# Kernel optimization log

Hardware: AMD Instinct MI355X
Metric: run time of the kernel (lower is better)

Reference implementation:

```python
import jax, jax.numpy as jnp
import numpy as np

B, T, C = 16, 1024, 128  # batch, block_size (window length), n_hembd


def setup_inputs() -> dict:
    key = jax.random.key(0)
    k1, k2, k3 = jax.random.split(key, 3)
    Q = jax.random.normal(k1, (B, T, C), dtype=jnp.float32)
    K = jax.random.normal(k2, (B, 2 * T - 1, C), dtype=jnp.float32)
    # learned parameter keyWindowBias: (1, 1, n_hembd, block_size)
    bias = jax.random.normal(k3, (1, 1, C, T), dtype=jnp.float32)
    return {"Q": Q, "K": K, "bias": bias}


def reference(Q, K, bias):
    # Original: K_sw = K.unfold(1, T, 1) -> (B, T, C, T) with K_sw[b,w,c,t] = K[b,w+t,c]
    #           Z = einsum('bwc,bwct->bwt', Q, K_sw + bias)
    # Distribute the dot product over the bias add to avoid materializing (B,T,C,T):
    #   Z[b,w,t] = sum_c Q[b,w,c] * K[b,w+t,c]  +  sum_c Q[b,w,c] * bias[c,t]
    Bn, Tn, Cn = Q.shape
    # Dense scores against all 2T-1 key positions: (B, T, 2T-1)
    S = jnp.einsum('bwc,bkc->bwk', Q, K)
    # Gather sliding-window diagonals: idx[w, t] = w + t
    idx = jnp.arange(Tn)[:, None] + jnp.arange(Tn)[None, :]  # (T, T)
    Zk = jnp.take_along_axis(S, idx[None, :, :], axis=2)      # (B, T, T)
    # Bias contribution: Q @ bias, shared across windows
    Zb = jnp.einsum('bwc,ct->bwt', Q, bias[0, 0])             # (B, T, T)
    return Zk + Zb
```

## Files before the change

kernel.cpp:

```cpp
#include <hip/hip_runtime.h>
#include <hip/hip_bf16.h>


#define B_    16
#define T_    1024
#define C_    128
#define KT_   2047

#define BW    32
#define BT    64
#define KROWS 96
#define SS_LD 98
#define LDB   136

#define LDSS  130

typedef unsigned short ushort_t;
typedef short bf16x8 __attribute__((ext_vector_type(8)));
typedef float f32x4  __attribute__((ext_vector_type(4)));

__device__ __forceinline__ unsigned short f2bf(float f) {
  unsigned int u = __float_as_uint(f);
  u += 0x7FFFu + ((u >> 16) & 1u);
  return (unsigned short)(u >> 16);
}

__device__ __forceinline__ bf16x8 pack8(float4 lo, float4 hi) {
  bf16x8 r;
  r[0] = (short)f2bf(lo.x); r[1] = (short)f2bf(lo.y);
  r[2] = (short)f2bf(lo.z); r[3] = (short)f2bf(lo.w);
  r[4] = (short)f2bf(hi.x); r[5] = (short)f2bf(hi.y);
  r[6] = (short)f2bf(hi.z); r[7] = (short)f2bf(hi.w);
  return r;
}

typedef const __attribute__((address_space(1))) unsigned int* gas_ptr;
typedef __attribute__((address_space(3))) unsigned int* las_ptr;
__device__ __forceinline__ void async_copy16(const void* g, void* l) {
  __builtin_amdgcn_global_load_lds((gas_ptr)g, (las_ptr)l, 16, 0, 0);
}

__device__ __forceinline__ const bf16x8* frag(const ushort_t* t, int row, int kc) {
  return (const bf16x8*)(t + (((row << 4) + (kc ^ (row & 7))) << 3));
}

#define KN4 1048064
#define BN4 32768

__global__ __launch_bounds__(256) void prepass(
    const float* __restrict__ K, const float* __restrict__ bias,
    ushort_t* __restrict__ Kb, ushort_t* __restrict__ bT) {
  int idx = blockIdx.x * 256 + threadIdx.x;
  if (idx < KN4) {
    float4 v = ((const float4*)K)[idx];
    ((ushort4*)Kb)[idx] = make_ushort4(f2bf(v.x), f2bf(v.y), f2bf(v.z), f2bf(v.w));
  } else {
    int i = idx - KN4;
    int c = i >> 8;
    int g = i & 255;
    float4 v = ((const float4*)(bias + c * T_))[g];
    int t = g << 2;
    bT[(t + 0) * C_ + c] = f2bf(v.x);
    bT[(t + 1) * C_ + c] = f2bf(v.y);
    bT[(t + 2) * C_ + c] = f2bf(v.z);
    bT[(t + 3) * C_ + c] = f2bf(v.w);
  }
}

__global__ __launch_bounds__(512) void swmm_main(
    const float* __restrict__ Q, const ushort_t* __restrict__ Kb,
    const ushort_t* __restrict__ bT, float* __restrict__ out) {
  __shared__ __align__(16) ushort_t tile[5120 * 8];
  __shared__ __align__(16) float Ss[64 * LDSS];

  const int b    = blockIdx.x;
  const int w0   = blockIdx.y * 64;
  const int tid  = threadIdx.x;
  const int wv   = tid >> 6;
  const int lane = tid & 63;
  const int frow = lane & 15;
  const int quad = lane >> 4;
  const int jb   = wv & 3;
  const int mg   = wv >> 2;

  const int r0 = tid >> 4;
  const int cc = (tid & 15) ^ (r0 & 7);
  const ushort_t* kbb = Kb + (size_t)b * KT_ * C_ + (cc << 3);
  const ushort_t* btb = bT + (cc << 3);

  auto stageK = [&](int chunk, int p) {
    int g0 = w0 + chunk * 64 + r0;
    int g1 = g0 + 32;
    if (g1 > KT_ - 1) g1 = KT_ - 1;
    async_copy16(kbb + (size_t)g0 * C_, &tile[(size_t)(p * 1024 + wv * 64) * 8]);
    async_copy16(kbb + (size_t)g1 * C_, &tile[(size_t)(p * 1024 + 512 + wv * 64) * 8]);
  };
  auto stageB = [&](int step, int q) {
    const ushort_t* g = btb + (size_t)(step * 64 + r0) * C_;
    async_copy16(g,           &tile[(size_t)(3072 + q * 1024 + wv * 64) * 8]);
    async_copy16(g + 32 * C_, &tile[(size_t)(3072 + q * 1024 + 512 + wv * 64) * 8]);
  };

  stageK(0, 0); stageK(1, 1); stageB(0, 0);

  bf16x8 a[4][4];
  {
    const float* qp = Q + ((size_t)(b * T_ + w0 + frow) << 7);
#pragma unroll
    for (int mi = 0; mi < 4; ++mi) {
      const float* qm = qp + ((size_t)(mi * 16) << 7);
#pragma unroll
      for (int kk = 0; kk < 4; ++kk) {
        int co = (kk * 4 + quad) << 3;
        float4 lo = *(const float4*)(qm + co);
        float4 hi = *(const float4*)(qm + co + 4);
        a[mi][kk] = pack8(lo, hi);
      }
    }
  }

  asm volatile("s_waitcnt vmcnt(0)" ::: "memory");
  __builtin_amdgcn_s_barrier();

  int p0 = 0, p1 = 1, p2 = 2;
  f32x4 baccA = {0.f, 0.f, 0.f, 0.f}, baccB = {0.f, 0.f, 0.f, 0.f};

  for (int s = 0; s < 16; ++s) {
    const int q0 = s & 1;

    if (s < 15) stageK(s + 2, p2);
    if (s < 15) stageB(s + 1, q0 ^ 1);

    __builtin_amdgcn_s_setprio(1);

    {
      const int n0 = wv * 16;
      const int pc = (wv >= 4) ? p1 : p0;
      const int lrow = pc * 64 + ((n0 + frow) & 63);
      f32x4 acc[4];
#pragma unroll
      for (int mi = 0; mi < 4; ++mi) acc[mi] = (f32x4){0.f, 0.f, 0.f, 0.f};
#pragma unroll
      for (int kk = 0; kk < 4; ++kk) {
        bf16x8 bb = *frag(tile, lrow, kk * 4 + quad);
#pragma unroll
        for (int mi = 0; mi < 4; ++mi)
          acc[mi] = __builtin_amdgcn_mfma_f32_16x16x32_bf16(a[mi][kk], bb, acc[mi], 0, 0, 0);
      }
#pragma unroll
      for (int mi = 0; mi < 4; ++mi)
#pragma unroll
        for (int r = 0; r < 4; ++r)
          Ss[(mi * 16 + quad * 4 + r) * LDSS + n0 + frow] = acc[mi][r];
    }

    {
      const int brow = 192 + q0 * 64 + jb * 16 + frow;
      f32x4 xA = {0.f, 0.f, 0.f, 0.f};
      f32x4 xB = {0.f, 0.f, 0.f, 0.f};
#pragma unroll
      for (int kk = 0; kk < 4; ++kk) {
        bf16x8 bb = *frag(tile, brow, kk * 4 + quad);
        xA = __builtin_amdgcn_mfma_f32_16x16x32_bf16(a[2 * mg + 0][kk], bb, xA, 0, 0, 0);
        xB = __builtin_amdgcn_mfma_f32_16x16x32_bf16(a[2 * mg + 1][kk], bb, xB, 0, 0, 0);
      }
      baccA = xA; baccB = xB;
    }

    __builtin_amdgcn_s_setprio(0);

    asm volatile("s_waitcnt lgkmcnt(0)" ::: "memory");
    __builtin_amdgcn_s_barrier();
    asm volatile("s_waitcnt vmcnt(0)" ::: "memory");

    {
      float* op = out + ((size_t)(b * T_ + w0) * T_) + s * 64 + jb * 16 + frow;
#pragma unroll
      for (int pi = 0; pi < 2; ++pi) {
        const int mi = 2 * mg + pi;
        const f32x4 acc = pi ? baccB : baccA;
#pragma unroll
        for (int r = 0; r < 4; ++r) {
          const int i = mi * 16 + quad * 4 + r;
          op[(size_t)i * T_] = acc[r] + Ss[i * LDSS + i + jb * 16 + frow];
        }
      }
    }
    asm volatile("s_waitcnt lgkmcnt(0)" ::: "memory");
    __builtin_amdgcn_s_barrier();

    const int tp = p0; p0 = p1; p1 = p2; p2 = tp;
  }
}

__global__ __launch_bounds__(256) void swmm_fallback(
    const float* __restrict__ Q, const float* __restrict__ K,
    const float* __restrict__ bias, float* __restrict__ out) {
  __shared__ __align__(16) unsigned short Qs[BW * LDB];
  __shared__ __align__(16) unsigned short Ks[KROWS * LDB];
  __shared__ __align__(16) unsigned short Bs[BT * LDB];
  __shared__ __align__(16) float Ssf[BW * SS_LD];

  const int b   = blockIdx.z;
  const int w0  = blockIdx.y * BW;
  const int t0  = blockIdx.x * BT;
  const int kbase = w0 + t0;
  const int tid = threadIdx.x;

  {
    const float4* src = (const float4*)(Q + (size_t)(b * T_ + w0) * C_);
    for (int v = tid; v < BW * (C_ / 4); v += 256) {
      int r = v >> 5, cc = v & 31;
      float4 q = src[r * 32 + cc];
      unsigned short* d = &Qs[r * LDB + (cc << 2)];
      d[0] = f2bf(q.x); d[1] = f2bf(q.y); d[2] = f2bf(q.z); d[3] = f2bf(q.w);
    }
  }
  {
    for (int v = tid; v < KROWS * (C_ / 4); v += 256) {
      int r = v >> 5, cc = v & 31;
      int g = kbase + r;
      float4 kv = make_float4(0.f, 0.f, 0.f, 0.f);
      if (g < KT_) kv = ((const float4*)(K + ((size_t)b * KT_ + g) * C_))[cc];
      unsigned short* d = &Ks[r * LDB + (cc << 2)];
      d[0] = f2bf(kv.x); d[1] = f2bf(kv.y); d[2] = f2bf(kv.z); d[3] = f2bf(kv.w);
    }
  }
  {
    for (int v = tid; v < C_ * (BT / 4); v += 256) {
      int c = v >> 4, jj = v & 15;
      float4 bv = ((const float4*)(bias + (size_t)c * T_ + t0))[jj];
      int j4 = jj << 2;
      Bs[(j4 + 0) * LDB + c] = f2bf(bv.x);
      Bs[(j4 + 1) * LDB + c] = f2bf(bv.y);
      Bs[(j4 + 2) * LDB + c] = f2bf(bv.z);
      Bs[(j4 + 3) * LDB + c] = f2bf(bv.w);
    }
  }
  __syncthreads();

  const int wv    = tid >> 6;
  const int lane  = tid & 63;
  const int frow  = lane & 15;
  const int koff  = (lane >> 4) * 8;
  const int drow4 = (lane >> 4) * 4;
  const int NS = KROWS / 16;

  for (int s = wv; s < 2 * NS; s += 4) {
    int mb = s / NS, nn = s % NS;
    int m0 = mb * 16, n0 = nn * 16;
    const unsigned short* arow = &Qs[(m0 + frow) * LDB + koff];
    const unsigned short* brow = &Ks[(n0 + frow) * LDB + koff];
    f32x4 acc = {0.f, 0.f, 0.f, 0.f};
#pragma unroll
    for (int k0 = 0; k0 < C_; k0 += 32) {
      bf16x8 a  = *(const bf16x8*)(arow + k0);
      bf16x8 bb = *(const bf16x8*)(brow + k0);
      acc = __builtin_amdgcn_mfma_f32_16x16x32_bf16(a, bb, acc, 0, 0, 0);
    }
#pragma unroll
    for (int r = 0; r < 4; ++r)
      Ssf[(m0 + drow4 + r) * SS_LD + n0 + frow] = acc[r];
  }

  f32x4 bacc[2];
#pragma unroll
  for (int q = 0; q < 2; ++q) {
    int idx = wv + q * 4;
    int m0 = (idx >> 2) * 16, jj0 = (idx & 3) * 16;
    const unsigned short* arow = &Qs[(m0 + frow) * LDB + koff];
    const unsigned short* brow = &Bs[(jj0 + frow) * LDB + koff];
    f32x4 acc = {0.f, 0.f, 0.f, 0.f};
#pragma unroll
    for (int k0 = 0; k0 < C_; k0 += 32) {
      bf16x8 a  = *(const bf16x8*)(arow + k0);
      bf16x8 bb = *(const bf16x8*)(brow + k0);
      acc = __builtin_amdgcn_mfma_f32_16x16x32_bf16(a, bb, acc, 0, 0, 0);
    }
    bacc[q] = acc;
  }
  __syncthreads();

#pragma unroll
  for (int q = 0; q < 2; ++q) {
    int idx = wv + q * 4;
    int m0 = (idx >> 2) * 16, jj0 = (idx & 3) * 16;
#pragma unroll
    for (int r = 0; r < 4; ++r) {
      int i = m0 + drow4 + r;
      int j = jj0 + frow;
      out[(size_t)(b * T_ + w0 + i) * T_ + t0 + j] = bacc[q][r] + Ssf[i * SS_LD + i + j];
    }
  }
}

extern "C" void kernel_launch(void* const* d_in, const int* in_sizes, int n_in,
                              void* d_out, int out_size, void* d_ws, size_t ws_size,
                              hipStream_t stream) {
  const float* Q    = (const float*)d_in[0];
  const float* K    = (const float*)d_in[1];
  const float* bias = (const float*)d_in[2];
  float* out = (float*)d_out;

  const size_t KB = (size_t)B_ * KT_ * C_ * 2;
  const size_t TB = (size_t)T_ * C_ * 2;

  if (ws_size >= KB + TB) {
    ushort_t* Kb = (ushort_t*)d_ws;
    ushort_t* bT = (ushort_t*)((char*)d_ws + KB);
    prepass<<<(KN4 + BN4) / 256, 256, 0, stream>>>(K, bias, Kb, bT);
    swmm_main<<<dim3(B_, T_ / 64), dim3(512), 0, stream>>>(Q, Kb, bT, out);
  } else {
    swmm_fallback<<<dim3(T_ / BT, T_ / BW, B_), dim3(256), 0, stream>>>(Q, K, bias, out);
  }
}
```

Baseline: 129.4 us.

## Stage bias scores in LDS for vectorized output stores and loosen vmcnt waits

The bias MFMA results are written to a new shared buffer, so each thread can emit contiguous float4 stores of 8 output values per row instead of scattered per-lane scalar stores. The wait on global loads moves to the top of each step using a partial vmcnt, which lets prefetches stay in flight across iterations, and the trailing barrier is removed. The intent is wider, coalesced output writes and better overlap of loads with compute. The cost is extra LDS traffic and footprint, plus a reliance on vmcnt counting, since the output stores also increment vmcnt, and on removing the final barrier, both of which risk correctness or hazards.

```diff
diff --git a/kernel.cpp b/kernel.cpp
--- a/kernel.cpp
+++ b/kernel.cpp
@@ -14,6 +14,7 @@
 #define LDB   136
 
 #define LDSS  130
+#define LDBS  65
 
 typedef unsigned short ushort_t;
 typedef short bf16x8 __attribute__((ext_vector_type(8)));
@@ -72,6 +73,7 @@
     const ushort_t* __restrict__ bT, float* __restrict__ out) {
   __shared__ __align__(16) ushort_t tile[5120 * 8];
   __shared__ __align__(16) float Ss[64 * LDSS];
+  __shared__ __align__(16) float Bss[64 * LDBS];
 
   const int b    = blockIdx.x;
   const int w0   = blockIdx.y * 64;
@@ -119,20 +121,25 @@
     }
   }
 
-  asm volatile("s_waitcnt vmcnt(0)" ::: "memory");
-  __builtin_amdgcn_s_barrier();
+  const int pi_row = tid >> 3;
+  const int pj0    = (tid & 7) * 8;
+  float* outb = out + ((size_t)(b * T_ + w0 + pi_row) * T_) + pj0;
 
   int p0 = 0, p1 = 1, p2 = 2;
-  f32x4 baccA = {0.f, 0.f, 0.f, 0.f}, baccB = {0.f, 0.f, 0.f, 0.f};
 
   for (int s = 0; s < 16; ++s) {
     const int q0 = s & 1;
 
-    if (s < 15) stageK(s + 2, p2);
-    if (s < 15) stageB(s + 1, q0 ^ 1);
+    if (s < 15) {
+      stageK(s + 2, p2);
+      stageB(s + 1, q0 ^ 1);
+    }
+    if (s < 15) asm volatile("s_waitcnt vmcnt(4)" ::: "memory");
+    else        asm volatile("s_waitcnt vmcnt(0)" ::: "memory");
+    __builtin_amdgcn_s_barrier();
+    __builtin_amdgcn_sched_barrier(0);
 
     __builtin_amdgcn_s_setprio(1);
-
     {
       const int n0 = wv * 16;
       const int pc = (wv >= 4) ? p1 : p0;
@@ -153,7 +160,6 @@
         for (int r = 0; r < 4; ++r)
           Ss[(mi * 16 + quad * 4 + r) * LDSS + n0 + frow] = acc[mi][r];
     }
-
     {
       const int brow = 192 + q0 * 64 + jb * 16 + frow;
       f32x4 xA = {0.f, 0.f, 0.f, 0.f};
@@ -164,30 +170,29 @@
         xA = __builtin_amdgcn_mfma_f32_16x16x32_bf16(a[2 * mg + 0][kk], bb, xA, 0, 0, 0);
         xB = __builtin_amdgcn_mfma_f32_16x16x32_bf16(a[2 * mg + 1][kk], bb, xB, 0, 0, 0);
       }
-      baccA = xA; baccB = xB;
-    }
-
+#pragma unroll
+      for (int r = 0; r < 4; ++r) {
+        Bss[((2 * mg + 0) * 16 + quad * 4 + r) * LDBS + jb * 16 + frow] = xA[r];
+        Bss[((2 * mg + 1) * 16 + quad * 4 + r) * LDBS + jb * 16 + frow] = xB[r];
+      }
+    }
     __builtin_amdgcn_s_setprio(0);
 
     asm volatile("s_waitcnt lgkmcnt(0)" ::: "memory");
     __builtin_amdgcn_s_barrier();
-    asm volatile("s_waitcnt vmcnt(0)" ::: "memory");
+    __builtin_amdgcn_sched_barrier(0);
 
     {
-      float* op = out + ((size_t)(b * T_ + w0) * T_) + s * 64 + jb * 16 + frow;
-#pragma unroll
-      for (int pi = 0; pi < 2; ++pi) {
-        const int mi = 2 * mg + pi;
-        const f32x4 acc = pi ? baccB : baccA;
-#pragma unroll
-        for (int r = 0; r < 4; ++r) {
-          const int i = mi * 16 + quad * 4 + r;
-          op[(size_t)i * T_] = acc[r] + Ss[i * LDSS + i + jb * 16 + frow];
-        }
-      }
+      float v[8];
+      const float* srow = &Ss[pi_row * LDSS + pi_row + pj0];
+      const float* brow2 = &Bss[pi_row * LDBS + pj0];
+#pragma unroll
+      for (int k = 0; k < 8; ++k) v[k] = srow[k] + brow2[k];
+      float4* dst = (float4*)(outb + (size_t)s * 64);
+      dst[0] = make_float4(v[0], v[1], v[2], v[3]);
+      dst[1] = make_float4(v[4], v[5], v[6], v[7]);
     }
     asm volatile("s_waitcnt lgkmcnt(0)" ::: "memory");
-    __builtin_amdgcn_s_barrier();
 
     const int tp = p0; p0 = p1; p1 = p2; p2 = tp;
   }
```

After: 147.9 us. 1.14x slower.

## Replace pipelined persistent-row kernel with small one-shot tiles and bf16 Q prepass

Applied to the files above, without the earlier changes.

The main kernel no longer has each 512-thread block walk all 16 t-chunks of a 64-row window with a triple-buffered async pipeline. Each 256-thread block now handles a 32x64 output tile: it loads Q, a 96-row K band and 64 bias rows in one async batch, runs both MFMA products, and writes the diagonal-gathered sum with float4 stores. Q is also converted to bf16 in the prepass, which adds one more global round trip. Blocks become shorter and far more numerous, giving better occupancy, but K and Q are reloaded per tile and there is no longer any load/compute overlap inside a block.

```diff
diff --git a/kernel.cpp b/kernel.cpp
--- a/kernel.cpp
+++ b/kernel.cpp
@@ -11,9 +11,7 @@
 #define BT    64
 #define KROWS 96
 #define SS_LD 98
-#define LDB   136
-
-#define LDSS  130
+#define LDBS2 68
 
 typedef unsigned short ushort_t;
 typedef short bf16x8 __attribute__((ext_vector_type(8)));
@@ -25,15 +23,6 @@
   return (unsigned short)(u >> 16);
 }
 
-__device__ __forceinline__ bf16x8 pack8(float4 lo, float4 hi) {
-  bf16x8 r;
-  r[0] = (short)f2bf(lo.x); r[1] = (short)f2bf(lo.y);
-  r[2] = (short)f2bf(lo.z); r[3] = (short)f2bf(lo.w);
-  r[4] = (short)f2bf(hi.x); r[5] = (short)f2bf(hi.y);
-  r[6] = (short)f2bf(hi.z); r[7] = (short)f2bf(hi.w);
-  return r;
-}
-
 typedef const __attribute__((address_space(1))) unsigned int* gas_ptr;
 typedef __attribute__((address_space(3))) unsigned int* las_ptr;
 __device__ __forceinline__ void async_copy16(const void* g, void* l) {
@@ -44,18 +33,24 @@
   return (const bf16x8*)(t + (((row << 4) + (kc ^ (row & 7))) << 3));
 }
 
+#define QN4 524288
 #define KN4 1048064
 #define BN4 32768
 
 __global__ __launch_bounds__(256) void prepass(
-    const float* __restrict__ K, const float* __restrict__ bias,
+    const float* __restrict__ Q, const float* __restrict__ K,
+    const float* __restrict__ bias, ushort_t* __restrict__ Qb,
     ushort_t* __restrict__ Kb, ushort_t* __restrict__ bT) {
   int idx = blockIdx.x * 256 + threadIdx.x;
-  if (idx < KN4) {
-    float4 v = ((const float4*)K)[idx];
-    ((ushort4*)Kb)[idx] = make_ushort4(f2bf(v.x), f2bf(v.y), f2bf(v.z), f2bf(v.w));
-  } else {
-    int i = idx - KN4;
+  if (idx < QN4) {
+    float4 v = ((const float4*)Q)[idx];
+    ((ushort4*)Qb)[idx] = make_ushort4(f2bf(v.x), f2bf(v.y), f2bf(v.z), f2bf(v.w));
+  } else if (idx < QN4 + KN4) {
+    int i = idx - QN4;
+    float4 v = ((const float4*)K)[i];
+    ((ushort4*)Kb)[i] = make_ushort4(f2bf(v.x), f2bf(v.y), f2bf(v.z), f2bf(v.w));
+  } else if (idx < QN4 + KN4 + BN4) {
+    int i = idx - (QN4 + KN4);
     int c = i >> 8;
     int g = i & 255;
     float4 v = ((const float4*)(bias + c * T_))[g];
@@ -67,132 +62,104 @@
   }
 }
 
-__global__ __launch_bounds__(512) void swmm_main(
-    const float* __restrict__ Q, const ushort_t* __restrict__ Kb,
+__global__ __launch_bounds__(256) void swmm_main(
+    const ushort_t* __restrict__ Qb, const ushort_t* __restrict__ Kb,
     const ushort_t* __restrict__ bT, float* __restrict__ out) {
-  __shared__ __align__(16) ushort_t tile[5120 * 8];
-  __shared__ __align__(16) float Ss[64 * LDSS];
-
-  const int b    = blockIdx.x;
-  const int w0   = blockIdx.y * 64;
-  const int tid  = threadIdx.x;
-  const int wv   = tid >> 6;
-  const int lane = tid & 63;
+  __shared__ __align__(16) ushort_t tile[3072 * 8];
+
+  const int b  = blockIdx.z;
+  const int w0 = blockIdx.y * BW;
+  const int t0 = blockIdx.x * BT;
+  const int kbase = w0 + t0;
+  const int tid = threadIdx.x;
+  const int wv = tid >> 6, lane = tid & 63;
+
+#pragma unroll
+  for (int seg = 0; seg < 12; ++seg) {
+    int slot = seg * 256 + tid;
+    int r = slot >> 4;
+    int c = (slot & 15) ^ (r & 7);
+    const ushort_t* g;
+    if (seg < 2) {
+      g = Qb + (((size_t)(b * T_ + w0 + r)) << 7) + (c << 3);
+    } else if (seg < 8) {
+      int gk = kbase + (r - 32);
+      if (gk > KT_ - 1) gk = KT_ - 1;
+      g = Kb + ((size_t)b * KT_ + gk) * C_ + (c << 3);
+    } else {
+      g = bT + (((size_t)(t0 + r - 128)) << 7) + (c << 3);
+    }
+    async_copy16(g, &tile[(size_t)(seg * 256 + wv * 64) * 8]);
+  }
+  __syncthreads();
+
   const int frow = lane & 15;
   const int quad = lane >> 4;
-  const int jb   = wv & 3;
-  const int mg   = wv >> 2;
-
-  const int r0 = tid >> 4;
-  const int cc = (tid & 15) ^ (r0 & 7);
-  const ushort_t* kbb = Kb + (size_t)b * KT_ * C_ + (cc << 3);
-  const ushort_t* btb = bT + (cc << 3);
-
-  auto stageK = [&](int chunk, int p) {
-    int g0 = w0 + chunk * 64 + r0;
-    int g1 = g0 + 32;
-    if (g1 > KT_ - 1) g1 = KT_ - 1;
-    async_copy16(kbb + (size_t)g0 * C_, &tile[(size_t)(p * 1024 + wv * 64) * 8]);
-    async_copy16(kbb + (size_t)g1 * C_, &tile[(size_t)(p * 1024 + 512 + wv * 64) * 8]);
-  };
-  auto stageB = [&](int step, int q) {
-    const ushort_t* g = btb + (size_t)(step * 64 + r0) * C_;
-    async_copy16(g,           &tile[(size_t)(3072 + q * 1024 + wv * 64) * 8]);
-    async_copy16(g + 32 * C_, &tile[(size_t)(3072 + q * 1024 + 512 + wv * 64) * 8]);
-  };
-
-  stageK(0, 0); stageK(1, 1); stageB(0, 0);
-
-  bf16x8 a[4][4];
-  {
-    const float* qp = Q + ((size_t)(b * T_ + w0 + frow) << 7);
-#pragma unroll
-    for (int mi = 0; mi < 4; ++mi) {
-      const float* qm = qp + ((size_t)(mi * 16) << 7);
-#pragma unroll
-      for (int kk = 0; kk < 4; ++kk) {
-        int co = (kk * 4 + quad) << 3;
-        float4 lo = *(const float4*)(qm + co);
-        float4 hi = *(const float4*)(qm + co + 4);
-        a[mi][kk] = pack8(lo, hi);
-      }
-    }
-  }
-
-  asm volatile("s_waitcnt vmcnt(0)" ::: "memory");
-  __builtin_amdgcn_s_barrier();
-
-  int p0 = 0, p1 = 1, p2 = 2;
-  f32x4 baccA = {0.f, 0.f, 0.f, 0.f}, baccB = {0.f, 0.f, 0.f, 0.f};
-
-  for (int s = 0; s < 16; ++s) {
-    const int q0 = s & 1;
-
-    if (s < 15) stageK(s + 2, p2);
-    if (s < 15) stageB(s + 1, q0 ^ 1);
-
-    __builtin_amdgcn_s_setprio(1);
-
-    {
-      const int n0 = wv * 16;
-      const int pc = (wv >= 4) ? p1 : p0;
-      const int lrow = pc * 64 + ((n0 + frow) & 63);
-      f32x4 acc[4];
-#pragma unroll
-      for (int mi = 0; mi < 4; ++mi) acc[mi] = (f32x4){0.f, 0.f, 0.f, 0.f};
-#pragma unroll
-      for (int kk = 0; kk < 4; ++kk) {
-        bf16x8 bb = *frag(tile, lrow, kk * 4 + quad);
-#pragma unroll
-        for (int mi = 0; mi < 4; ++mi)
-          acc[mi] = __builtin_amdgcn_mfma_f32_16x16x32_bf16(a[mi][kk], bb, acc[mi], 0, 0, 0);
-      }
-#pragma unroll
-      for (int mi = 0; mi < 4; ++mi)
-#pragma unroll
-        for (int r = 0; r < 4; ++r)
-          Ss[(mi * 16 + quad * 4 + r) * LDSS + n0 + frow] = acc[mi][r];
-    }
-
-    {
-      const int brow = 192 + q0 * 64 + jb * 16 + frow;
-      f32x4 xA = {0.f, 0.f, 0.f, 0.f};
-      f32x4 xB = {0.f, 0.f, 0.f, 0.f};
-#pragma unroll
-      for (int kk = 0; kk < 4; ++kk) {
-        bf16x8 bb = *frag(tile, brow, kk * 4 + quad);
-        xA = __builtin_amdgcn_mfma_f32_16x16x32_bf16(a[2 * mg + 0][kk], bb, xA, 0, 0, 0);
-        xB = __builtin_amdgcn_mfma_f32_16x16x32_bf16(a[2 * mg + 1][kk], bb, xB, 0, 0, 0);
-      }
-      baccA = xA; baccB = xB;
-    }
-
-    __builtin_amdgcn_s_setprio(0);
-
-    asm volatile("s_waitcnt lgkmcnt(0)" ::: "memory");
-    __builtin_amdgcn_s_barrier();
-    asm volatile("s_waitcnt vmcnt(0)" ::: "memory");
-
-    {
-      float* op = out + ((size_t)(b * T_ + w0) * T_) + s * 64 + jb * 16 + frow;
-#pragma unroll
-      for (int pi = 0; pi < 2; ++pi) {
-        const int mi = 2 * mg + pi;
-        const f32x4 acc = pi ? baccB : baccA;
-#pragma unroll
-        for (int r = 0; r < 4; ++r) {
-          const int i = mi * 16 + quad * 4 + r;
-          op[(size_t)i * T_] = acc[r] + Ss[i * LDSS + i + jb * 16 + frow];
-        }
-      }
-    }
-    asm volatile("s_waitcnt lgkmcnt(0)" ::: "memory");
-    __builtin_amdgcn_s_barrier();
-
-    const int tp = p0; p0 = p1; p1 = p2; p2 = tp;
-  }
-}
-
+  const int drow4 = quad * 4;
+
+  f32x4 bacc[2];
+#pragma unroll
+  for (int q = 0; q < 2; ++q) {
+    int idx = wv + q * 4;
+    int m0 = (idx >> 2) * 16, j0 = (idx & 3) * 16;
+    f32x4 acc = {0.f, 0.f, 0.f, 0.f};
+#pragma unroll
+    for (int kk = 0; kk < 4; ++kk) {
+      int kc = kk * 4 + quad;
+      bf16x8 a  = *frag(tile, m0 + frow, kc);
+      bf16x8 bb = *frag(tile, 128 + j0 + frow, kc);
+      acc = __builtin_amdgcn_mfma_f32_16x16x32_bf16(a, bb, acc, 0, 0, 0);
+    }
+    bacc[q] = acc;
+  }
+  __syncthreads();
+
+  float* Ss = (float*)&tile[2048 * 8];
+#pragma unroll
+  for (int q = 0; q < 3; ++q) {
+    int s = wv + q * 4;
+    int mb = s / 6, nn = s % 6;
+    int m0 = mb * 16, n0 = nn * 16;
+    f32x4 acc = {0.f, 0.f, 0.f, 0.f};
+#pragma unroll
+    for (int kk = 0; kk < 4; ++kk) {
+      int kc = kk * 4 + quad;
+      bf16x8 a  = *frag(tile, m0 + frow, kc);
+      bf16x8 bb = *frag(tile, 32 + n0 + frow, kc);
+      acc = __builtin_amdgcn_mfma_f32_16x16x32_bf16(a, bb, acc, 0, 0, 0);
+    }
+#pragma unroll
+    for (int r = 0; r < 4; ++r)
+      Ss[(m0 + drow4 + r) * SS_LD + n0 + frow] = acc[r];
+  }
+  __syncthreads();
+
+  float* Bss = (float*)&tile[4096];
+#pragma unroll
+  for (int q = 0; q < 2; ++q) {
+    int idx = wv + q * 4;
+    int m0 = (idx >> 2) * 16, j0 = (idx & 3) * 16;
+#pragma unroll
+    for (int r = 0; r < 4; ++r)
+      Bss[(m0 + drow4 + r) * LDBS2 + j0 + frow] = bacc[q][r];
+  }
+  __syncthreads();
+
+  {
+    const int pi  = tid >> 3;
+    const int pj0 = (tid & 7) * 8;
+    float v[8];
+    const float* srow = &Ss[pi * SS_LD + pi + pj0];
+    const float* brow = &Bss[pi * LDBS2 + pj0];
+#pragma unroll
+    for (int k = 0; k < 8; ++k) v[k] = srow[k] + brow[k];
+    float4* dst = (float4*)(out + (size_t)(b * T_ + w0 + pi) * T_ + t0 + pj0);
+    dst[0] = make_float4(v[0], v[1], v[2], v[3]);
+    dst[1] = make_float4(v[4], v[5], v[6], v[7]);
+  }
+}
+
+#define LDB 136
 __global__ __launch_bounds__(256) void swmm_fallback(
     const float* __restrict__ Q, const float* __restrict__ K,
     const float* __restrict__ bias, float* __restrict__ out) {
@@ -267,9 +234,9 @@
 #pragma unroll
   for (int q = 0; q < 2; ++q) {
     int idx = wv + q * 4;
-    int m0 = (idx >> 2) * 16, jj0 = (idx & 3) * 16;
+    int m0 = (idx >> 2) * 16, j0 = (idx & 3) * 16;
     const unsigned short* arow = &Qs[(m0 + frow) * LDB + koff];
-    const unsigned short* brow = &Bs[(jj0 + frow) * LDB + koff];
+    const unsigned short* brow = &Bs[(j0 + frow) * LDB + koff];
     f32x4 acc = {0.f, 0.f, 0.f, 0.f};
 #pragma unroll
     for (int k0 = 0; k0 < C_; k0 += 32) {
@@ -284,11 +251,11 @@
 #pragma unroll
   for (int q = 0; q < 2; ++q) {
     int idx = wv + q * 4;
-    int m0 = (idx >> 2) * 16, jj0 = (idx & 3) * 16;
+    int m0 = (idx >> 2) * 16, j0 = (idx & 3) * 16;
 #pragma unroll
     for (int r = 0; r < 4; ++r) {
       int i = m0 + drow4 + r;
-      int j = jj0 + frow;
+      int j = j0 + frow;
       out[(size_t)(b * T_ + w0 + i) * T_ + t0 + j] = bacc[q][r] + Ssf[i * SS_LD + i + j];
     }
   }
@@ -302,15 +269,18 @@
   const float* bias = (const float*)d_in[2];
   float* out = (float*)d_out;
 
+  const size_t QB = (size_t)B_ * T_ * C_ * 2;
   const size_t KB = (size_t)B_ * KT_ * C_ * 2;
   const size_t TB = (size_t)T_ * C_ * 2;
-
-  if (ws_size >= KB + TB) {
-    ushort_t* Kb = (ushort_t*)d_ws;
-    ushort_t* bT = (ushort_t*)((char*)d_ws + KB);
-    prepass<<<(KN4 + BN4) / 256, 256, 0, stream>>>(K, bias, Kb, bT);
-    swmm_main<<<dim3(B_, T_ / 64), dim3(512), 0, stream>>>(Q, Kb, bT, out);
+  dim3 grid(T_ / BT, T_ / BW, B_);
+
+  if (ws_size >= QB + KB + TB) {
+    ushort_t* Qb = (ushort_t*)d_ws;
+    ushort_t* Kb = (ushort_t*)((char*)d_ws + QB);
+    ushort_t* bT = (ushort_t*)((char*)d_ws + QB + KB);
+    prepass<<<(QN4 + KN4 + BN4) / 256, 256, 0, stream>>>(Q, K, bias, Qb, Kb, bT);
+    swmm_main<<<grid, dim3(256), 0, stream>>>(Qb, Kb, bT, out);
   } else {
-    swmm_fallback<<<dim3(T_ / BT, T_ / BW, B_), dim3(256), 0, stream>>>(Q, K, bias, out);
-  }
-}
+    swmm_fallback<<<grid, dim3(256), 0, stream>>>(Q, K, bias, out);
+  }
+}
```

Measured after the change: 123.0 us. 1.05x faster.
